# Optimization experiments

Hardware: AMD Instinct MI355X
Metric: run time of the kernel (lower is better)

## Reference

```python
import jax, jax.numpy as jnp
import numpy as np

FLOOR = 1e-06
B, T, C = 64, 4096, 80


def _ema(x, w):
    """EMA a_t = w*x_t + (1-w)*a_{t-1}, a_{-1} = x[:,0], via parallel associative scan.
    x: [B,T,C], w: [C] (clipped to [0,1]). Returns [B,T,C].
    Note: with init = x[:,0], the first output is exactly x[:,0].
    """
    A = jnp.broadcast_to(1.0 - w, x.shape)          # decay per step
    b = w * x                                        # input injection per step
    # Fold the initial state into step 0: a_0 = w*x_0 + (1-w)*x_0 = x_0
    A = A.at[:, 0, :].set(0.0)
    b = b.at[:, 0, :].set(x[:, 0, :])

    def combine(c1, c2):
        A1, b1 = c1
        A2, b2 = c2
        return A1 * A2, A2 * b1 + b2

    _, ema = jax.lax.associative_scan(combine, (A, b), axis=1)
    return ema


def setup_inputs() -> dict:
    key = jax.random.key(0)
    k_in, = jax.random.split(key, 1)
    inputs = jax.random.uniform(k_in, (B, T, C), dtype=jnp.float32)  # non-negative energies
    alpha = jnp.full((C,), 0.96, dtype=jnp.float32)
    delta = jnp.full((C,), 2.0, dtype=jnp.float32)
    root = jnp.full((C,), 2.0, dtype=jnp.float32)
    smooth = jnp.full((C,), 0.04, dtype=jnp.float32)
    return {"inputs": inputs, "alpha": alpha, "delta": delta, "root": root, "smooth": smooth}


def reference(inputs, alpha, delta, root, smooth):
    w = jnp.clip(smooth, 0.0, 1.0)
    a = jnp.minimum(alpha, 1.0)
    r = jnp.maximum(root, 1.0)
    ema_smoother = _ema(inputs, w)                       # [B,T,C]
    one_over_root = 1.0 / r                              # [C]
    out = (inputs / (FLOOR + ema_smoother) ** a + delta) ** one_over_root - delta ** one_over_root
    return out
```

## Files before the change

kernel.cpp:

```cpp
#include <hip/hip_runtime.h>

#define FLOOR_EPS 1e-6f

constexpr int Bn    = 64;
constexpr int Tn    = 4096;
constexpr int Cn    = 80;
constexpr int G     = Cn / 4;
constexpr int CHUNK = 32;
constexpr int NCH   = Tn / CHUNK;
constexpr int TOT   = Bn * NCH * G;

__global__ __launch_bounds__(256)
void pcen_sum_kernel(const float* __restrict__ x,
                     const float* __restrict__ smooth,
                     float4* __restrict__ ws_sum) {
    int tid = blockIdx.x * blockDim.x + threadIdx.x;
    if (tid >= TOT) return;
    int g = tid % G;
    int k = (tid / G) % NCH;
    int b = tid / (G * NCH);

    float4 smv = ((const float4*)smooth)[g];
    float w0 = fminf(fmaxf(smv.x, 0.f), 1.f), w1 = fminf(fmaxf(smv.y, 0.f), 1.f);
    float w2 = fminf(fmaxf(smv.z, 0.f), 1.f), w3 = fminf(fmaxf(smv.w, 0.f), 1.f);
    float d0 = 1.f - w0, d1 = 1.f - w1, d2 = 1.f - w2, d3 = 1.f - w3;

    const float4* px = (const float4*)x + ((size_t)b * Tn + (size_t)k * CHUNK) * G + g;
    float4 xs[CHUNK];
    #pragma unroll
    for (int u = 0; u < CHUNK; ++u) xs[u] = px[(size_t)u * G];

    float e0, e1, e2, e3;
    if (k == 0) { e0 = xs[0].x; e1 = xs[0].y; e2 = xs[0].z; e3 = xs[0].w; }
    else        { e0 = 0.f; e1 = 0.f; e2 = 0.f; e3 = 0.f; }
    #pragma unroll
    for (int u = 0; u < CHUNK; ++u) {
        e0 = fmaf(d0, e0, w0 * xs[u].x);
        e1 = fmaf(d1, e1, w1 * xs[u].y);
        e2 = fmaf(d2, e2, w2 * xs[u].z);
        e3 = fmaf(d3, e3, w3 * xs[u].w);
    }
    ws_sum[tid] = make_float4(e0, e1, e2, e3);
}

__global__ __launch_bounds__(NCH)
void pcen_chunkscan_kernel(const float* __restrict__ smooth,
                           float4* __restrict__ ws_sum) {
    __shared__ float4 sc[2][NCH];
    const int k = threadIdx.x;
    const int g = blockIdx.x % G;
    const int b = blockIdx.x / G;

    float4 smv = ((const float4*)smooth)[g];
    float W[4];
    {
        float ws4[4] = {smv.x, smv.y, smv.z, smv.w};
        #pragma unroll
        for (int j = 0; j < 4; ++j) {
            float d = 1.f - fminf(fmaxf(ws4[j], 0.f), 1.f);
            float d2 = d * d, d4 = d2 * d2, d8 = d4 * d4, d16 = d8 * d8;
            W[j] = d16 * d16;
        }
    }

    const size_t idx = ((size_t)b * NCH + k) * G + g;
    sc[0][k] = ws_sum[idx];
    __syncthreads();
    int src = 0;
    float W0 = W[0], W1 = W[1], W2 = W[2], W3 = W[3];
    #pragma unroll
    for (int off = 1; off < NCH; off <<= 1) {
        float4 v = sc[src][k];
        if (k >= off) {
            float4 u = sc[src][k - off];
            v.x = fmaf(W0, u.x, v.x);
            v.y = fmaf(W1, u.y, v.y);
            v.z = fmaf(W2, u.z, v.z);
            v.w = fmaf(W3, u.w, v.w);
        }
        sc[src ^ 1][k] = v;
        __syncthreads();
        src ^= 1;
        W0 *= W0; W1 *= W1; W2 *= W2; W3 *= W3;
    }
    ws_sum[idx] = sc[src][k];
}

__global__ __launch_bounds__(256)
void pcen_out_kernel(const float* __restrict__ x,
                     const float* __restrict__ alpha,
                     const float* __restrict__ delta,
                     const float* __restrict__ root,
                     const float* __restrict__ smooth,
                     const float4* __restrict__ ws_scan,
                     float* __restrict__ out) {
    int tid = blockIdx.x * blockDim.x + threadIdx.x;
    if (tid >= TOT) return;
    int g = tid % G;
    int k = (tid / G) % NCH;
    int b = tid / (G * NCH);

    float4 smv = ((const float4*)smooth)[g];
    float4 alv = ((const float4*)alpha)[g];
    float4 rov = ((const float4*)root)[g];
    float4 dlv = ((const float4*)delta)[g];
    float w[4], dcy[4], nega[4], invr[4], dl[4], sub[4];
    {
        float ws4[4] = {smv.x, smv.y, smv.z, smv.w};
        float as[4]  = {alv.x, alv.y, alv.z, alv.w};
        float rs[4]  = {rov.x, rov.y, rov.z, rov.w};
        dl[0]=dlv.x; dl[1]=dlv.y; dl[2]=dlv.z; dl[3]=dlv.w;
        #pragma unroll
        for (int j = 0; j < 4; ++j) {
            w[j]    = fminf(fmaxf(ws4[j], 0.f), 1.f);
            dcy[j]  = 1.f - w[j];
            nega[j] = -fminf(as[j], 1.f);
            invr[j] = 1.f / fmaxf(rs[j], 1.f);
            sub[j]  = __expf(invr[j] * __logf(dl[j]));
        }
    }
    bool all_sqrt = (invr[0] == 0.5f) & (invr[1] == 0.5f) &
                    (invr[2] == 0.5f) & (invr[3] == 0.5f);

    const float4* px = (const float4*)x + ((size_t)b * Tn + (size_t)k * CHUNK) * G + g;
    float4* po = (float4*)out + ((size_t)b * Tn + (size_t)k * CHUNK) * G + g;

    float m0, m1, m2, m3;
    float4 xs[CHUNK];
    if (k > 0) {
        float4 s = ws_scan[tid - G];
        #pragma unroll
        for (int u = 0; u < CHUNK; ++u) xs[u] = px[(size_t)u * G];
        m0 = s.x; m1 = s.y; m2 = s.z; m3 = s.w;
    } else {
        #pragma unroll
        for (int u = 0; u < CHUNK; ++u) xs[u] = px[(size_t)u * G];
        m0 = xs[0].x; m1 = xs[0].y; m2 = xs[0].z; m3 = xs[0].w;
    }

    if (all_sqrt) {
        #pragma unroll
        for (int u = 0; u < CHUNK; ++u) {
            float4 xv = xs[u];
            m0 = fmaf(dcy[0], m0, w[0] * xv.x);
            m1 = fmaf(dcy[1], m1, w[1] * xv.y);
            m2 = fmaf(dcy[2], m2, w[2] * xv.z);
            m3 = fmaf(dcy[3], m3, w[3] * xv.w);
            float4 ov;
            ov.x = sqrtf(fmaf(xv.x, __expf(nega[0] * __logf(FLOOR_EPS + m0)), dl[0])) - sub[0];
            ov.y = sqrtf(fmaf(xv.y, __expf(nega[1] * __logf(FLOOR_EPS + m1)), dl[1])) - sub[1];
            ov.z = sqrtf(fmaf(xv.z, __expf(nega[2] * __logf(FLOOR_EPS + m2)), dl[2])) - sub[2];
            ov.w = sqrtf(fmaf(xv.w, __expf(nega[3] * __logf(FLOOR_EPS + m3)), dl[3])) - sub[3];
            po[(size_t)u * G] = ov;
        }
    } else {
        #pragma unroll
        for (int u = 0; u < CHUNK; ++u) {
            float4 xv = xs[u];
            float xv4[4] = {xv.x, xv.y, xv.z, xv.w};
            float mm[4]  = {m0, m1, m2, m3};
            float os[4];
            #pragma unroll
            for (int j = 0; j < 4; ++j) {
                mm[j]   = fmaf(dcy[j], mm[j], w[j] * xv4[j]);
                float p = __expf(nega[j] * __logf(FLOOR_EPS + mm[j]));
                float v = fmaf(xv4[j], p, dl[j]);
                os[j]   = __expf(invr[j] * __logf(v)) - sub[j];
            }
            m0 = mm[0]; m1 = mm[1]; m2 = mm[2]; m3 = mm[3];
            po[(size_t)u * G] = make_float4(os[0], os[1], os[2], os[3]);
        }
    }
}

extern "C" void kernel_launch(void* const* d_in, const int* in_sizes, int n_in,
                              void* d_out, int out_size, void* d_ws, size_t ws_size,
                              hipStream_t stream) {
    const float* x      = (const float*)d_in[0];
    const float* alpha  = (const float*)d_in[1];
    const float* delta  = (const float*)d_in[2];
    const float* root   = (const float*)d_in[3];
    const float* smooth = (const float*)d_in[4];
    float* out = (float*)d_out;

    float4* ws_sum = (float4*)d_ws;

    int block = 256;
    int gridA = (TOT + block - 1) / block;
    pcen_sum_kernel<<<gridA, block, 0, stream>>>(x, smooth, ws_sum);
    pcen_chunkscan_kernel<<<Bn * G, NCH, 0, stream>>>(smooth, ws_sum);
    pcen_out_kernel<<<gridA, block, 0, stream>>>(x, alpha, delta, root, smooth,
                                                 ws_sum, out);
}
```

Measured before the change: 182.8 us.

## Fuse three-pass chunked EMA scan into single kernel with decoupled lookback

```diff
diff --git a/kernel.cpp b/kernel.cpp
--- a/kernel.cpp
+++ b/kernel.cpp
@@ -2,150 +2,151 @@
 
 #define FLOOR_EPS 1e-6f
 
-constexpr int Bn    = 64;
-constexpr int Tn    = 4096;
-constexpr int Cn    = 80;
-constexpr int G     = Cn / 4;
-constexpr int CHUNK = 32;
-constexpr int NCH   = Tn / CHUNK;
-constexpr int TOT   = Bn * NCH * G;
+constexpr int Bn   = 64;
+constexpr int Tn   = 4096;
+constexpr int Cn   = 80;
+constexpr int G    = Cn / 4;
+constexpr int P    = 16;
+constexpr int SLAB = Tn / P;
+constexpr int KC   = 16;
+constexpr int CH   = SLAB / KC;
+constexpr int NT   = KC * G;
 
-__global__ __launch_bounds__(256)
-void pcen_sum_kernel(const float* __restrict__ x,
-                     const float* __restrict__ smooth,
-                     float4* __restrict__ ws_sum) {
-    int tid = blockIdx.x * blockDim.x + threadIdx.x;
-    if (tid >= TOT) return;
-    int g = tid % G;
-    int k = (tid / G) % NCH;
-    int b = tid / (G * NCH);
+__global__ __launch_bounds__(NT, 5)
+void pcen_fused(const float* __restrict__ x,
+                const float* __restrict__ alpha,
+                const float* __restrict__ delta,
+                const float* __restrict__ root,
+                const float* __restrict__ smooth,
+                float4* __restrict__ partial,
+                int*    __restrict__ flags,
+                float*  __restrict__ out)
+{
+    __shared__ float4 sc[2][KC][G];
 
-    float4 smv = ((const float4*)smooth)[g];
+    const int p  = blockIdx.x % P;
+    const int b  = blockIdx.x / P;
+    const int t  = threadIdx.x;
+    const int g  = t % G;
+    const int kc = t / G;
+
+    const float4 smv = ((const float4*)smooth)[g];
     float w0 = fminf(fmaxf(smv.x, 0.f), 1.f), w1 = fminf(fmaxf(smv.y, 0.f), 1.f);
     float w2 = fminf(fmaxf(smv.z, 0.f), 1.f), w3 = fminf(fmaxf(smv.w, 0.f), 1.f);
     float d0 = 1.f - w0, d1 = 1.f - w1, d2 = 1.f - w2, d3 = 1.f - w3;
 
-    const float4* px = (const float4*)x + ((size_t)b * Tn + (size_t)k * CHUNK) * G + g;
-    float4 xs[CHUNK];
+    float q0 = d0 * d0, q1 = d1 * d1, q2 = d2 * d2, q3 = d3 * d3;
+    q0 *= q0; q1 *= q1; q2 *= q2; q3 *= q3;
+    q0 *= q0; q1 *= q1; q2 *= q2; q3 *= q3;
+    q0 *= q0; q1 *= q1; q2 *= q2; q3 *= q3;
+
+    const size_t rowbase = ((size_t)b * Tn + (size_t)p * SLAB + (size_t)kc * CH) * G + g;
+    const float4* px = (const float4*)x + rowbase;
+
+    const bool fc = (p == 0) && (kc == 0);
+    float e0, e1, e2, e3;
+    if (fc) { float4 v = px[0]; e0 = v.x; e1 = v.y; e2 = v.z; e3 = v.w; }
+    else    { e0 = 0.f; e1 = 0.f; e2 = 0.f; e3 = 0.f; }
     #pragma unroll
-    for (int u = 0; u < CHUNK; ++u) xs[u] = px[(size_t)u * G];
+    for (int u = 0; u < CH; ++u) {
+        float4 v = px[(size_t)u * G];
+        e0 = fmaf(d0, e0, w0 * v.x);
+        e1 = fmaf(d1, e1, w1 * v.y);
+        e2 = fmaf(d2, e2, w2 * v.z);
+        e3 = fmaf(d3, e3, w3 * v.w);
+    }
+    sc[0][kc][g] = make_float4(e0, e1, e2, e3);
+    __syncthreads();
 
-    float e0, e1, e2, e3;
-    if (k == 0) { e0 = xs[0].x; e1 = xs[0].y; e2 = xs[0].z; e3 = xs[0].w; }
-    else        { e0 = 0.f; e1 = 0.f; e2 = 0.f; e3 = 0.f; }
+    float W0 = q0, W1 = q1, W2 = q2, W3 = q3;
+    int src = 0;
     #pragma unroll
-    for (int u = 0; u < CHUNK; ++u) {
-        e0 = fmaf(d0, e0, w0 * xs[u].x);
-        e1 = fmaf(d1, e1, w1 * xs[u].y);
-        e2 = fmaf(d2, e2, w2 * xs[u].z);
-        e3 = fmaf(d3, e3, w3 * xs[u].w);
-    }
-    ws_sum[tid] = make_float4(e0, e1, e2, e3);
-}
-
-__global__ __launch_bounds__(NCH)
-void pcen_chunkscan_kernel(const float* __restrict__ smooth,
-                           float4* __restrict__ ws_sum) {
-    __shared__ float4 sc[2][NCH];
-    const int k = threadIdx.x;
-    const int g = blockIdx.x % G;
-    const int b = blockIdx.x / G;
-
-    float4 smv = ((const float4*)smooth)[g];
-    float W[4];
-    {
-        float ws4[4] = {smv.x, smv.y, smv.z, smv.w};
-        #pragma unroll
-        for (int j = 0; j < 4; ++j) {
-            float d = 1.f - fminf(fmaxf(ws4[j], 0.f), 1.f);
-            float d2 = d * d, d4 = d2 * d2, d8 = d4 * d4, d16 = d8 * d8;
-            W[j] = d16 * d16;
+    for (int off = 1; off < KC; off <<= 1) {
+        float4 v = sc[src][kc][g];
+        if (kc >= off) {
+            float4 u4 = sc[src][kc - off][g];
+            v.x = fmaf(W0, u4.x, v.x);
+            v.y = fmaf(W1, u4.y, v.y);
+            v.z = fmaf(W2, u4.z, v.z);
+            v.w = fmaf(W3, u4.w, v.w);
         }
-    }
-
-    const size_t idx = ((size_t)b * NCH + k) * G + g;
-    sc[0][k] = ws_sum[idx];
-    __syncthreads();
-    int src = 0;
-    float W0 = W[0], W1 = W[1], W2 = W[2], W3 = W[3];
-    #pragma unroll
-    for (int off = 1; off < NCH; off <<= 1) {
-        float4 v = sc[src][k];
-        if (k >= off) {
-            float4 u = sc[src][k - off];
-            v.x = fmaf(W0, u.x, v.x);
-            v.y = fmaf(W1, u.y, v.y);
-            v.z = fmaf(W2, u.z, v.z);
-            v.w = fmaf(W3, u.w, v.w);
-        }
-        sc[src ^ 1][k] = v;
+        sc[src ^ 1][kc][g] = v;
         __syncthreads();
         src ^= 1;
         W0 *= W0; W1 *= W1; W2 *= W2; W3 *= W3;
     }
-    ws_sum[idx] = sc[src][k];
-}
 
-__global__ __launch_bounds__(256)
-void pcen_out_kernel(const float* __restrict__ x,
-                     const float* __restrict__ alpha,
-                     const float* __restrict__ delta,
-                     const float* __restrict__ root,
-                     const float* __restrict__ smooth,
-                     const float4* __restrict__ ws_scan,
-                     float* __restrict__ out) {
-    int tid = blockIdx.x * blockDim.x + threadIdx.x;
-    if (tid >= TOT) return;
-    int g = tid % G;
-    int k = (tid / G) % NCH;
-    int b = tid / (G * NCH);
+    if (kc == KC - 1) {
+        partial[(size_t)blockIdx.x * G + g] = sc[src][kc][g];
+        __threadfence();
+    }
+    __syncthreads();
+    if (t == 0)
+        __hip_atomic_store(&flags[blockIdx.x], 1, __ATOMIC_RELEASE,
+                           __HIP_MEMORY_SCOPE_AGENT);
 
-    float4 smv = ((const float4*)smooth)[g];
-    float4 alv = ((const float4*)alpha)[g];
-    float4 rov = ((const float4*)root)[g];
-    float4 dlv = ((const float4*)delta)[g];
-    float w[4], dcy[4], nega[4], invr[4], dl[4], sub[4];
+    float S0 = 0.f, S1 = 0.f, S2 = 0.f, S3 = 0.f;
+    const int fb = b * P;
+    for (int q = 0; q < p; ++q) {
+        while (__hip_atomic_load(&flags[fb + q], __ATOMIC_ACQUIRE,
+                                 __HIP_MEMORY_SCOPE_AGENT) == 0)
+            __builtin_amdgcn_s_sleep(2);
+        float4 bq = partial[(size_t)(fb + q) * G + g];
+        S0 = fmaf(W0, S0, bq.x);
+        S1 = fmaf(W1, S1, bq.y);
+        S2 = fmaf(W2, S2, bq.z);
+        S3 = fmaf(W3, S3, bq.w);
+    }
+
+    float m0, m1, m2, m3;
+    if (kc == 0) {
+        m0 = S0; m1 = S1; m2 = S2; m3 = S3;
+    } else {
+        float4 ex = sc[src][kc - 1][g];
+        float k0 = 1.f, k1 = 1.f, k2 = 1.f, k3 = 1.f;
+        float b0 = q0, b1 = q1, b2 = q2, b3 = q3;
+        int kk = kc;
+        #pragma unroll
+        for (int bit = 0; bit < 4; ++bit) {
+            if (kk & 1) { k0 *= b0; k1 *= b1; k2 *= b2; k3 *= b3; }
+            b0 *= b0; b1 *= b1; b2 *= b2; b3 *= b3;
+            kk >>= 1;
+        }
+        m0 = fmaf(k0, S0, ex.x);
+        m1 = fmaf(k1, S1, ex.y);
+        m2 = fmaf(k2, S2, ex.z);
+        m3 = fmaf(k3, S3, ex.w);
+    }
+    if (fc) { float4 v = px[0]; m0 = v.x; m1 = v.y; m2 = v.z; m3 = v.w; }
+
+    const float4 alv = ((const float4*)alpha)[g];
+    const float4 dlv = ((const float4*)delta)[g];
+    const float4 rov = ((const float4*)root)[g];
+    float nega[4], invr[4], dl[4], sub[4];
     {
-        float ws4[4] = {smv.x, smv.y, smv.z, smv.w};
-        float as[4]  = {alv.x, alv.y, alv.z, alv.w};
-        float rs[4]  = {rov.x, rov.y, rov.z, rov.w};
-        dl[0]=dlv.x; dl[1]=dlv.y; dl[2]=dlv.z; dl[3]=dlv.w;
+        float as[4] = {alv.x, alv.y, alv.z, alv.w};
+        float rs[4] = {rov.x, rov.y, rov.z, rov.w};
+        dl[0] = dlv.x; dl[1] = dlv.y; dl[2] = dlv.z; dl[3] = dlv.w;
         #pragma unroll
         for (int j = 0; j < 4; ++j) {
-            w[j]    = fminf(fmaxf(ws4[j], 0.f), 1.f);
-            dcy[j]  = 1.f - w[j];
             nega[j] = -fminf(as[j], 1.f);
             invr[j] = 1.f / fmaxf(rs[j], 1.f);
             sub[j]  = __expf(invr[j] * __logf(dl[j]));
         }
     }
-    bool all_sqrt = (invr[0] == 0.5f) & (invr[1] == 0.5f) &
-                    (invr[2] == 0.5f) & (invr[3] == 0.5f);
+    const bool all_sqrt = (invr[0] == 0.5f) & (invr[1] == 0.5f) &
+                          (invr[2] == 0.5f) & (invr[3] == 0.5f);
 
-    const float4* px = (const float4*)x + ((size_t)b * Tn + (size_t)k * CHUNK) * G + g;
-    float4* po = (float4*)out + ((size_t)b * Tn + (size_t)k * CHUNK) * G + g;
-
-    float m0, m1, m2, m3;
-    float4 xs[CHUNK];
-    if (k > 0) {
-        float4 s = ws_scan[tid - G];
-        #pragma unroll
-        for (int u = 0; u < CHUNK; ++u) xs[u] = px[(size_t)u * G];
-        m0 = s.x; m1 = s.y; m2 = s.z; m3 = s.w;
-    } else {
-        #pragma unroll
-        for (int u = 0; u < CHUNK; ++u) xs[u] = px[(size_t)u * G];
-        m0 = xs[0].x; m1 = xs[0].y; m2 = xs[0].z; m3 = xs[0].w;
-    }
+    float4* po = (float4*)out + rowbase;
 
     if (all_sqrt) {
         #pragma unroll
-        for (int u = 0; u < CHUNK; ++u) {
-            float4 xv = xs[u];
-            m0 = fmaf(dcy[0], m0, w[0] * xv.x);
-            m1 = fmaf(dcy[1], m1, w[1] * xv.y);
-            m2 = fmaf(dcy[2], m2, w[2] * xv.z);
-            m3 = fmaf(dcy[3], m3, w[3] * xv.w);
+        for (int u = 0; u < CH; ++u) {
+            float4 xv = px[(size_t)u * G];
+            m0 = fmaf(d0, m0, w0 * xv.x);
+            m1 = fmaf(d1, m1, w1 * xv.y);
+            m2 = fmaf(d2, m2, w2 * xv.z);
+            m3 = fmaf(d3, m3, w3 * xv.w);
             float4 ov;
             ov.x = sqrtf(fmaf(xv.x, __expf(nega[0] * __logf(FLOOR_EPS + m0)), dl[0])) - sub[0];
             ov.y = sqrtf(fmaf(xv.y, __expf(nega[1] * __logf(FLOOR_EPS + m1)), dl[1])) - sub[1];
@@ -154,20 +155,20 @@
             po[(size_t)u * G] = ov;
         }
     } else {
+        float w[4] = {w0, w1, w2, w3}, dc[4] = {d0, d1, d2, d3};
+        float mm[4] = {m0, m1, m2, m3};
         #pragma unroll
-        for (int u = 0; u < CHUNK; ++u) {
-            float4 xv = xs[u];
+        for (int u = 0; u < CH; ++u) {
+            float4 xv = px[(size_t)u * G];
             float xv4[4] = {xv.x, xv.y, xv.z, xv.w};
-            float mm[4]  = {m0, m1, m2, m3};
             float os[4];
             #pragma unroll
             for (int j = 0; j < 4; ++j) {
-                mm[j]   = fmaf(dcy[j], mm[j], w[j] * xv4[j]);
-                float p = __expf(nega[j] * __logf(FLOOR_EPS + mm[j]));
-                float v = fmaf(xv4[j], p, dl[j]);
-                os[j]   = __expf(invr[j] * __logf(v)) - sub[j];
+                mm[j]   = fmaf(dc[j], mm[j], w[j] * xv4[j]);
+                float pw = __expf(nega[j] * __logf(FLOOR_EPS + mm[j]));
+                float v  = fmaf(xv4[j], pw, dl[j]);
+                os[j]    = __expf(invr[j] * __logf(v)) - sub[j];
             }
-            m0 = mm[0]; m1 = mm[1]; m2 = mm[2]; m3 = mm[3];
             po[(size_t)u * G] = make_float4(os[0], os[1], os[2], os[3]);
         }
     }
@@ -183,12 +184,10 @@
     const float* smooth = (const float*)d_in[4];
     float* out = (float*)d_out;
 
-    float4* ws_sum = (float4*)d_ws;
+    float4* partial = (float4*)d_ws;
+    int*    flags   = (int*)((char*)d_ws + sizeof(float4) * Bn * P * G);
 
-    int block = 256;
-    int gridA = (TOT + block - 1) / block;
-    pcen_sum_kernel<<<gridA, block, 0, stream>>>(x, smooth, ws_sum);
-    pcen_chunkscan_kernel<<<Bn * G, NCH, 0, stream>>>(smooth, ws_sum);
-    pcen_out_kernel<<<gridA, block, 0, stream>>>(x, alpha, delta, root, smooth,
-                                                 ws_sum, out);
+    hipMemsetAsync(flags, 0, sizeof(int) * Bn * P, stream);
+    pcen_fused<<<Bn * P, NT, 0, stream>>>(x, alpha, delta, root, smooth,
+                                          partial, flags, out);
 }
```

After: 622.7 us. 3.41x slower.
